# Optimization experiments

Measured on AMD Instinct MI355X. Metric: run time of the kernel, lower is better.

## Reference

```python
import jax, jax.numpy as jnp
import numpy as np

VOCAB = 50257
CUTOFF = (10000, 50000, 50257)  # cutoff + [vocab_size] per __init__
D = 1024
B, T = 2, 1024
HEAD_SZ = CUTOFF[0] + 2  # cutoff[0] + n_tail_clusters


def setup_inputs() -> dict:
    key = jax.random.key(0)
    ks = jax.random.split(key, 7)
    def xavier(k, shp):
        # xavier_uniform as in init_weights
        bound = np.sqrt(6.0 / (shp[0] + shp[1])).astype(np.float32)
        return jax.random.uniform(k, shp, dtype=jnp.float32, minval=-bound, maxval=bound)
    return {
        "input": jax.random.normal(ks[0], (B, T, D), dtype=jnp.float32),
        "target": jax.random.randint(ks[1], (B, T), 0, VOCAB),
        "head_w": xavier(ks[2], (HEAD_SZ, D)),              # [10002, 1024]
        "t0_a": xavier(ks[3], (D, D)),                       # [1024, 1024]
        "t0_b": xavier(ks[4], (CUTOFF[1] - CUTOFF[0], D)),   # [40000, 1024]
        "t1_a": xavier(ks[5], (D // 4, D)),                  # [256, 1024]
        "t1_b": xavier(ks[6], (CUTOFF[2] - CUTOFF[1], D // 4)),  # [207, 256]
    }


def reference(input, target, head_w, t0_a, t0_b, t1_a, t1_b):
    # Faithful jax version of AdaptiveSoftmax.get_log_prob (eval mode, dropout=0).
    # Torch updates log_probs[idxs, start:end] only for rows whose target lies in
    # cluster i (leaving other rows zero); we express the same gather->small GEMM
    # chain->log_softmax->prior-add->scatter via masked writes (jit-friendly).
    bsz, length, dim = input.shape
    xi = input.reshape(-1, dim)                     # [N, D]
    tgt = target.reshape(-1)                        # [N]

    head_lp = jax.nn.log_softmax(xi @ head_w.T, axis=1)        # [N, HEAD_SZ]
    tail_priors = head_lp[:, CUTOFF[0] - 1:HEAD_SZ - 1]        # [N, 2]

    log_probs = jnp.zeros((xi.shape[0], VOCAB), dtype=input.dtype)
    log_probs = log_probs.at[:, :HEAD_SZ].set(head_lp)

    tails = ((t0_a, t0_b), (t1_a, t1_b))
    for i, (wa, wb) in enumerate(tails):
        lo, hi = CUTOFF[i], CUTOFF[i + 1]
        mask = (tgt >= lo) & (tgt < hi)                        # [N]
        # Linear(D, D//4**i) -> Linear(D//4**i, hi-lo), then log_softmax + prior
        tail_lp = jax.nn.log_softmax((xi @ wa.T) @ wb.T, axis=1) + tail_priors[:, i:i + 1]
        log_probs = log_probs.at[:, lo:hi].set(
            jnp.where(mask[:, None], tail_lp, log_probs[:, lo:hi]))
    return log_probs.reshape(bsz, length, VOCAB)
```

## Files before the change

### kernel.cpp

```cpp
#include <hip/hip_runtime.h>

typedef unsigned short u16;
typedef unsigned int u32;
typedef __attribute__((ext_vector_type(4))) float f32x4;
typedef __bf16 bf16x8 __attribute__((ext_vector_type(8)));
typedef __attribute__((ext_vector_type(8))) unsigned short u16x8;

__device__ __forceinline__ u16 f2bf(float x) {
    u32 u = __builtin_bit_cast(u32, x);
    u += 0x7FFFu + ((u >> 16) & 1u);
    return (u16)(u >> 16);
}
__device__ __forceinline__ float bf2f(u16 u) {
    return __builtin_bit_cast(float, ((u32)u) << 16);
}
__device__ __forceinline__ void gld_lds16(void* lds, const void* g) {
    __builtin_amdgcn_global_load_lds(
        (const __attribute__((address_space(1))) void*)g,
        (__attribute__((address_space(3))) void*)lds, 16, 0, 0);
}

__device__ __forceinline__ size_t pack_base_tail(long row) {
    return (size_t)row * 100514 + 59936 - ((row * 2) & 7);
}
__device__ __forceinline__ size_t pack_base_head(long row) {
    return (size_t)row * 100514 + 20480 - ((row * 2) & 7);
}

__global__ __launch_bounds__(256) void cvt_all(const float* __restrict__ x,
                                               const float* __restrict__ hw,
                                               const float* __restrict__ t0a,
                                               const float* __restrict__ t1a,
                                               const float* __restrict__ t0b,
                                               const float* __restrict__ t1b,
                                               u16* __restrict__ XI, u16* __restrict__ HW,
                                               u16* __restrict__ TAB, u16* __restrict__ T0B,
                                               u16* __restrict__ T1B) {
    int b = blockIdx.x;
    const float* src; u16* dst; int n, b0, nb;
    if (b < 80)        { src = x;    dst = XI;            n = 2097152;  b0 = 0;    nb = 80;   }
    else if (b < 472)  { src = hw;   dst = HW;            n = 10242048; b0 = 80;   nb = 392;  }
    else if (b < 512)  { src = t0a;  dst = TAB;           n = 1048576;  b0 = 472;  nb = 40;   }
    else if (b < 522)  { src = t1a;  dst = TAB + 1048576; n = 262144;   b0 = 512;  nb = 10;   }
    else if (b < 2086) { src = t0b;  dst = T0B;           n = 40960000; b0 = 522;  nb = 1564; }
    else if (b < 2090) { src = t1b;  dst = T1B;           n = 65792;    b0 = 2086; nb = 4;    }
    else if (b < 2100) { src = 0;    dst = HW + 10242048; n = 243712;   b0 = 2090; nb = 10;   }
    else               { src = 0;    dst = T0B + 40960000; n = 196608;  b0 = 2100; nb = 8;    }
    int i0 = (b - b0) * 1024 + threadIdx.x * 4;
    int stride = nb * 1024;
    if (src) {
        for (int i = i0; i < n; i += stride) {
            float4 v = *(const float4*)(src + i);
            ushort4 o;
            o.x = f2bf(v.x); o.y = f2bf(v.y); o.z = f2bf(v.z); o.w = f2bf(v.w);
            *(ushort4*)(dst + i) = o;
        }
    } else {
        ushort4 z = {0, 0, 0, 0};
        for (int i = i0; i < n; i += stride) *(ushort4*)(dst + i) = z;
    }
}

__global__ __launch_bounds__(256) void build_map(const int* __restrict__ tgt,
                                                 int* __restrict__ rowlist,
                                                 int* __restrict__ cntbuf) {
    __shared__ int cs[257];
    __shared__ int fu[256];
    int t = threadIdx.x;
    int cnt_local = 0, first_un = 1 << 30;
    int mk[8];
#pragma unroll
    for (int k = 0; k < 8; k++) {
        int r = t * 8 + k;
        int tg = tgt[r];
        int m = (tg >= 10000 && tg < 50000) ? 1 : 0;
        mk[k] = m;
        cnt_local += m;
        if (!m && first_un == (1 << 30)) first_un = r;
    }
    cs[t + 1] = cnt_local;
    fu[t] = first_un;
    __syncthreads();
    if (t == 0) {
        cs[0] = 0;
        for (int i = 1; i <= 256; i++) cs[i] += cs[i - 1];
        int d = 1 << 30;
        for (int i = 0; i < 256; i++) d = min(d, fu[i]);
        if (d == (1 << 30)) d = 0;
        int cnt = cs[256];
        cntbuf[0] = cnt;
        cntbuf[1] = (cnt + 255) & ~255;
        cntbuf[2] = d;
    }
    __syncthreads();
    int off = cs[t];
#pragma unroll
    for (int k = 0; k < 8; k++)
        if (mk[k]) rowlist[off++] = t * 8 + k;
    int cnt = cs[256], cntp = (cnt + 255) & ~255, d = cntbuf[2];
    for (int j = cnt + t; j < cntp; j += 256) rowlist[j] = d;
}

template <int TAIL>
__global__ __launch_bounds__(512, 2) void gemm256(const u16* __restrict__ A,
                                                  const u16* __restrict__ B,
                                                  u16* __restrict__ outpk,
                                                  const int* __restrict__ rowlist,
                                                  const int* __restrict__ cntbuf,
                                                  float* __restrict__ part) {
    const int m0 = blockIdx.x * 256, n0 = blockIdx.y * 256;
    if (TAIL) { if (m0 >= cntbuf[1]) return; }
    __shared__ u16 lds[4][16384];
    const int tid = threadIdx.x;
    const int lane = tid & 63, wv = tid >> 6;
    const int wm = wv >> 2, wn = wv & 3;
    const int lr = lane & 15, hi = lane >> 4;

    const int c0 = tid, c1 = 512 + tid;
    int ga0 = m0 + ((c0 >> 6) << 4) + (c0 & 15);
    int ga1 = m0 + ((c1 >> 6) << 4) + (c1 & 15);
    const u16* sA0;
    const u16* sA1;
    if (TAIL) {
        sA0 = A + (size_t)rowlist[ga0] * 1280 + ((c0 >> 4) & 3) * 8;
        sA1 = A + (size_t)rowlist[ga1] * 1280 + ((c1 >> 4) & 3) * 8;
    } else {
        sA0 = A + (size_t)ga0 * 1024 + ((c0 >> 4) & 3) * 8;
        sA1 = A + (size_t)ga1 * 1024 + ((c1 >> 4) & 3) * 8;
    }
    const u16* sB0 = B + (size_t)(n0 + ((c0 >> 6) << 4) + (c0 & 15)) * 1024 + ((c0 >> 4) & 3) * 8;
    const u16* sB1 = B + (size_t)(n0 + ((c1 >> 6) << 4) + (c1 & 15)) * 1024 + ((c1 >> 4) & 3) * 8;

    f32x4 acc[8][4] = {};

    auto stage = [&](int buf, int kt) {
        char* d = (char*)&lds[buf][0] + tid * 16;
        gld_lds16(d,          sA0 + kt);
        gld_lds16(d + 8192,   sA1 + kt);
        gld_lds16(d + 16384,  sB0 + kt);
        gld_lds16(d + 24576,  sB1 + kt);
    };
    auto compute = [&](int buf) {
        const u16* LA = &lds[buf][0];
        const u16* LB = &lds[buf][8192];
        bf16x8 bfr[4];
#pragma unroll
        for (int j = 0; j < 4; j++)
            bfr[j] = *(const bf16x8*)(LB + (wn * 4 + j) * 512 + hi * 128 + lr * 8);
        __builtin_amdgcn_s_setprio(1);
#pragma unroll
        for (int m = 0; m < 8; m++) {
            bf16x8 af = *(const bf16x8*)(LA + (wm * 8 + m) * 512 + hi * 128 + lr * 8);
#pragma unroll
            for (int j = 0; j < 4; j++)
                acc[m][j] = __builtin_amdgcn_mfma_f32_16x16x32_bf16(af, bfr[j], acc[m][j], 0, 0, 0);
        }
        __builtin_amdgcn_s_setprio(0);
    };

    stage(0, 0);
    stage(1, 32);
    asm volatile("s_waitcnt vmcnt(4)" ::: "memory");
    __builtin_amdgcn_s_barrier();
#pragma unroll 1
    for (int t = 0; t < 30; ++t) {
        stage((t + 2) & 3, (t + 2) * 32);
        compute(t & 3);
        asm volatile("s_waitcnt vmcnt(4)" ::: "memory");
        __builtin_amdgcn_s_barrier();
    }
    compute(2);
    asm volatile("s_waitcnt vmcnt(0)" ::: "memory");
    __builtin_amdgcn_s_barrier();
    compute(3);

    const int cr = hi * 4, cc = lr;
    const int climit = TAIL ? 40000 : 10002;
    const int pstride = TAIL ? 628 : 160;
#pragma unroll
    for (int m = 0; m < 8; m++) {
#pragma unroll
        for (int q = 0; q < 4; q++) {
            int r = m0 + wm * 128 + m * 16 + cr + q;
            long orow = TAIL ? rowlist[r] : r;
            size_t base = TAIL ? pack_base_tail(orow) : pack_base_head(orow);
            u16* dst = outpk + base + n0 + wn * 64 + cc;
            float s = 0.f;
#pragma unroll
            for (int j = 0; j < 4; j++) {
                float v = acc[m][j][q];
                dst[j * 16] = f2bf(v);
                int col = n0 + wn * 64 + j * 16 + cc;
                s += (col < climit) ? __expf(v) : 0.f;
            }
            s += __shfl_xor(s, 1); s += __shfl_xor(s, 2);
            s += __shfl_xor(s, 4); s += __shfl_xor(s, 8);
            if (cc == 0) part[(size_t)r * pstride + (n0 >> 6) + wn] = s;
        }
    }
}

__global__ __launch_bounds__(256) void gemm_nt_bf16(const u16* __restrict__ A, int lda,
                                                    const u16* __restrict__ B, int ldb,
                                                    u16* __restrict__ Cb, long ldc, int K) {
    __shared__ u16 lA[128 * 32];
    __shared__ u16 lB[128 * 32];
    const int tid = threadIdx.x;
    const int lane = tid & 63, wv = tid >> 6;
    const int m0 = blockIdx.x * 128, n0 = blockIdx.y * 128;

    const u16* gA0 = A + (size_t)(m0 + (tid >> 2)) * lda + (tid & 3) * 8;
    const u16* gB0 = B + (size_t)(n0 + (tid >> 2)) * ldb + (tid & 3) * 8;
    char* dA = (char*)lA + wv * 1024;
    char* dB = (char*)lB + wv * 1024;

    f32x4 acc[4][4] = {};
    const int wm = wv >> 1, wn = wv & 1;
    const int lr = lane & 15;
    const int lk = (lane >> 4) * 8;

    for (int kt = 0; kt < K; kt += 32) {
        __syncthreads();
        gld_lds16(dA, gA0);
        gld_lds16(dA + 4096, gA0 + 64 * (size_t)lda);
        gld_lds16(dB, gB0);
        gld_lds16(dB + 4096, gB0 + 64 * (size_t)ldb);
        gA0 += 32; gB0 += 32;
        __syncthreads();

        bf16x8 af[4], bfr[4];
#pragma unroll
        for (int i = 0; i < 4; i++) {
            af[i]  = *(const bf16x8*)(lA + (wm * 64 + i * 16 + lr) * 32 + lk);
            bfr[i] = *(const bf16x8*)(lB + (wn * 64 + i * 16 + lr) * 32 + lk);
        }
#pragma unroll
        for (int i = 0; i < 4; i++)
#pragma unroll
            for (int j = 0; j < 4; j++)
                acc[i][j] = __builtin_amdgcn_mfma_f32_16x16x32_bf16(af[i], bfr[j], acc[i][j], 0, 0, 0);
    }

    const int cr = (lane >> 4) * 4;
    const int cc = lane & 15;
#pragma unroll
    for (int i = 0; i < 4; i++) {
        int rbase = m0 + wm * 64 + i * 16 + cr;
#pragma unroll
        for (int j = 0; j < 4; j++) {
            int c = n0 + wn * 64 + j * 16 + cc;
#pragma unroll
            for (int q = 0; q < 4; q++)
                Cb[(size_t)(rbase + q) * (size_t)ldc + c] = f2bf(acc[i][j][q]);
        }
    }
}

__global__ __launch_bounds__(256) void head_norm(float* __restrict__ out,
                                                 float* __restrict__ stats,
                                                 const float* __restrict__ parth) {
    const int row = blockIdx.x, tid = threadIdx.x;
    float s = (tid < 160) ? parth[(size_t)row * 160 + tid] : 0.f;
#pragma unroll
    for (int o = 32; o; o >>= 1) s += __shfl_xor(s, o);
    __shared__ float red[4];
    if ((tid & 63) == 0) red[tid >> 6] = s;
    __syncthreads();
    float logZ = __logf(red[0] + red[1] + red[2] + red[3]);
    const u16* pk = (const u16*)out + pack_base_head(row);
    float* p = out + (size_t)row * 50257;
    for (int k = 0; k < 5; k++) {
        int c0 = k * 2048 + tid * 8;
        if (c0 + 8 <= 10002) {
            u16x8 xv = *(const u16x8*)(pk + c0);
#pragma unroll
            for (int z = 0; z < 8; z++) p[c0 + z] = bf2f(xv[z]) - logZ;
        } else if (c0 < 10002) {
            for (int z = 0; c0 + z < 10002; z++) p[c0 + z] = bf2f(pk[c0 + z]) - logZ;
        }
    }
    if (tid == 0) {
        float* st = stats + row * 8;
        float l0 = bf2f(pk[9999]) - logZ;
        float l1 = bf2f(pk[10000]) - logZ;
        float l2 = bf2f(pk[10001]) - logZ;
        st[0] = l0; st[1] = l1; st[2] = l1; st[3] = l2;
    }
}

__global__ __launch_bounds__(256) void reduce_t0(const float* __restrict__ part,
                                                 const int* __restrict__ rowlist,
                                                 const int* __restrict__ cntbuf,
                                                 const float* __restrict__ ST,
                                                 float* __restrict__ FA) {
    int r = blockIdx.x;
    if (r >= cntbuf[0]) return;
    int tid = threadIdx.x;
    float s = 0.f;
    for (int c = tid; c < 628; c += 256) s += part[(size_t)r * 628 + c];
#pragma unroll
    for (int o = 32; o; o >>= 1) s += __shfl_xor(s, o);
    __shared__ float red[4];
    if ((tid & 63) == 0) red[tid >> 6] = s;
    __syncthreads();
    if (tid == 0) {
        float S = red[0] + red[1] + red[2] + red[3];
        int orow = rowlist[r];
        FA[orow] = __logf(S) - ST[orow * 8 + 0];
    }
}

__global__ __launch_bounds__(256) void tail0_norm(float* __restrict__ out,
                                                  const int* __restrict__ tgt,
                                                  const float* __restrict__ ST,
                                                  const float* __restrict__ FA) {
    const int row = blockIdx.x, tid = threadIdx.x;
    float* p = out + (size_t)row * 50257 + 10000;
    int t = tgt[row];
    if (t >= 10000 && t < 50000) {
        float A = FA[row];
        const u16* src = (const u16*)out + pack_base_tail(row);
        for (int k = 0; k < 5; k++) {
            float v[4][8];
#pragma unroll
            for (int g = 0; g < 4; g++) {
                int o = 2048 * g + tid * 8;
                if (o < 8000) {
                    u16x8 xv = *(const u16x8*)(src + 8000 * k + o);
#pragma unroll
                    for (int z = 0; z < 8; z++) v[g][z] = bf2f(xv[z]);
                }
            }
            __syncthreads();
#pragma unroll
            for (int g = 0; g < 4; g++) {
                int o = 2048 * g + tid * 8;
                if (o < 8000) {
                    int e = 8000 * k + o;
#pragma unroll
                    for (int z = 0; z < 8; z++) p[e + z] = v[g][z] - A;
                }
            }
            __syncthreads();
        }
    } else {
        float v0 = ST[row * 8 + 2], v1 = ST[row * 8 + 3];
        for (int e = tid; e < 40000; e += 256) p[e] = 0.f;
        if (tid == 0) { p[0] = v0; p[1] = v1; }
    }
}

__global__ __launch_bounds__(256) void tail1_kernel(float* __restrict__ out,
                                                    const int* __restrict__ tgt,
                                                    const u16* __restrict__ proj,
                                                    const u16* __restrict__ t1b,
                                                    const float* __restrict__ stats) {
    const int row = blockIdx.x, tid = threadIdx.x;
    float* p = out + (size_t)row * 50257 + 50000;
    int t = tgt[row];
    if (t < 50000) {
        for (int c = tid; c < 257; c += 256) p[c] = 0.f;
        return;
    }
    __shared__ float pr[256];
    __shared__ float lg[257];
    __shared__ float red[4];
    pr[tid] = bf2f(proj[(size_t)row * 1280 + 1024 + tid]);
    __syncthreads();
    for (int c = tid; c < 257; c += 256) {
        const u16* w = t1b + c * 256;
        float acc = 0.f;
        for (int k = 0; k < 256; k++) acc += bf2f(w[k]) * pr[k];
        lg[c] = acc;
    }
    __syncthreads();
    float s = 0.f;
    for (int c = tid; c < 257; c += 256) s += __expf(lg[c]);
#pragma unroll
    for (int o = 32; o; o >>= 1) s += __shfl_xor(s, o);
    if ((tid & 63) == 0) red[tid >> 6] = s;
    __syncthreads();
    float A = __logf(red[0] + red[1] + red[2] + red[3]) - stats[row * 8 + 1];
    for (int c = tid; c < 257; c += 256) p[c] = lg[c] - A;
}

#define OFF_XI    0UL
#define OFF_HEADW 4194304UL
#define OFF_TAB   25165824UL
#define OFF_T0B   27787264UL
#define OFF_T1B   110100480UL
#define OFF_PROJ  110232064UL
#define OFF_ST    115474944UL
#define OFF_PART  115540480UL
#define OFF_PARTH 120685056UL
#define OFF_FA    121995776UL
#define OFF_MAP   122003968UL
#define OFF_CNT   122012160UL

extern "C" void kernel_launch(void* const* d_in, const int* in_sizes, int n_in,
                              void* d_out, int out_size, void* d_ws, size_t ws_size,
                              hipStream_t stream) {
    const float* x   = (const float*)d_in[0];
    const int*   tgt = (const int*)d_in[1];
    const float* hw  = (const float*)d_in[2];
    const float* t0a = (const float*)d_in[3];
    const float* t0b = (const float*)d_in[4];
    const float* t1a = (const float*)d_in[5];
    const float* t1b = (const float*)d_in[6];
    float* out = (float*)d_out;
    char* ws = (char*)d_ws;

    u16* XI     = (u16*)(ws + OFF_XI);
    u16* HW     = (u16*)(ws + OFF_HEADW);
    u16* TAB    = (u16*)(ws + OFF_TAB);
    u16* T0B    = (u16*)(ws + OFF_T0B);
    u16* T1B    = (u16*)(ws + OFF_T1B);
    u16* PROJ   = (u16*)(ws + OFF_PROJ);
    float* ST   = (float*)(ws + OFF_ST);
    float* PART = (float*)(ws + OFF_PART);
    float* PARTH = (float*)(ws + OFF_PARTH);
    float* FA   = (float*)(ws + OFF_FA);
    int* MAP    = (int*)(ws + OFF_MAP);
    int* CNT    = (int*)(ws + OFF_CNT);

    cvt_all<<<2108, 256, 0, stream>>>(x, hw, t0a, t1a, t0b, t1b, XI, HW, TAB, T0B, T1B);

    build_map<<<1, 256, 0, stream>>>(tgt, MAP, CNT);

    gemm256<0><<<dim3(8, 40), 512, 0, stream>>>(XI, HW, (u16*)d_out, nullptr, nullptr, PARTH);

    head_norm<<<2048, 256, 0, stream>>>(out, ST, PARTH);

    gemm_nt_bf16<<<dim3(16, 10), 256, 0, stream>>>(XI, 1024, TAB, 1024, PROJ, 1280L, 1024);

    gemm256<1><<<dim3(8, 157), 512, 0, stream>>>(PROJ, T0B, (u16*)d_out, MAP, CNT, PART);

    reduce_t0<<<2048, 256, 0, stream>>>(PART, MAP, CNT, ST, FA);
    tail0_norm<<<2048, 256, 0, stream>>>(out, tgt, ST, FA);

    tail1_kernel<<<2048, 256, 0, stream>>>(out, tgt, PROJ, T1B, ST);
}
```

Baseline: 558.1 us.

## Interleave LDS reads, global loads and MFMA phases; fuse tail0 reduce into norm

The GEMM main loop is split into two half-phases, each fenced by scheduling barriers. A and B tile loads are issued separately and interleaved with LDS fragment reads and MFMA groups, so memory traffic overlaps compute at a finer grain. The build_map kernel now lists all rows, masked rows first and unmasked rows after, in place of padding with a dummy row. This lets reduce_t0 be merged into tail0_norm, which indexes through the row list and drops one launch and the FA buffer. The extra barriers add synchronisation points and the register pressure may change.

```diff
diff --git a/kernel.cpp b/kernel.cpp
--- a/kernel.cpp
+++ b/kernel.cpp
@@ -65,41 +65,35 @@
                                                  int* __restrict__ rowlist,
                                                  int* __restrict__ cntbuf) {
     __shared__ int cs[257];
-    __shared__ int fu[256];
     int t = threadIdx.x;
-    int cnt_local = 0, first_un = 1 << 30;
+    int cnt_local = 0;
     int mk[8];
 #pragma unroll
     for (int k = 0; k < 8; k++) {
-        int r = t * 8 + k;
-        int tg = tgt[r];
-        int m = (tg >= 10000 && tg < 50000) ? 1 : 0;
-        mk[k] = m;
-        cnt_local += m;
-        if (!m && first_un == (1 << 30)) first_un = r;
+        int tg = tgt[t * 8 + k];
+        mk[k] = (tg >= 10000 && tg < 50000) ? 1 : 0;
+        cnt_local += mk[k];
     }
     cs[t + 1] = cnt_local;
-    fu[t] = first_un;
     __syncthreads();
     if (t == 0) {
         cs[0] = 0;
         for (int i = 1; i <= 256; i++) cs[i] += cs[i - 1];
-        int d = 1 << 30;
-        for (int i = 0; i < 256; i++) d = min(d, fu[i]);
-        if (d == (1 << 30)) d = 0;
-        int cnt = cs[256];
-        cntbuf[0] = cnt;
-        cntbuf[1] = (cnt + 255) & ~255;
-        cntbuf[2] = d;
-    }
-    __syncthreads();
-    int off = cs[t];
-#pragma unroll
-    for (int k = 0; k < 8; k++)
-        if (mk[k]) rowlist[off++] = t * 8 + k;
-    int cnt = cs[256], cntp = (cnt + 255) & ~255, d = cntbuf[2];
-    for (int j = cnt + t; j < cntp; j += 256) rowlist[j] = d;
-}
+        cntbuf[0] = cs[256];
+        cntbuf[1] = (cs[256] + 255) & ~255;
+    }
+    __syncthreads();
+    int cnt = cs[256];
+    int offm = cs[t];
+    int offu = cnt + (t * 8 - cs[t]);
+#pragma unroll
+    for (int k = 0; k < 8; k++) {
+        if (mk[k]) rowlist[offm++] = t * 8 + k;
+        else       rowlist[offu++] = t * 8 + k;
+    }
+}
+
+#define PH_BAR() do { __builtin_amdgcn_sched_barrier(0); __builtin_amdgcn_s_barrier(); __builtin_amdgcn_sched_barrier(0); } while (0)
 
 template <int TAIL>
 __global__ __launch_bounds__(512, 2) void gemm256(const u16* __restrict__ A,
@@ -132,47 +126,82 @@
     const u16* sB1 = B + (size_t)(n0 + ((c1 >> 6) << 4) + (c1 & 15)) * 1024 + ((c1 >> 4) & 3) * 8;
 
     f32x4 acc[8][4] = {};
-
-    auto stage = [&](int buf, int kt) {
+    bf16x8 Bf[4], Af[4];
+
+    auto stageA = [&](int buf, int kt) {
         char* d = (char*)&lds[buf][0] + tid * 16;
-        gld_lds16(d,          sA0 + kt);
-        gld_lds16(d + 8192,   sA1 + kt);
-        gld_lds16(d + 16384,  sB0 + kt);
-        gld_lds16(d + 24576,  sB1 + kt);
+        gld_lds16(d,        sA0 + kt);
+        gld_lds16(d + 8192, sA1 + kt);
     };
-    auto compute = [&](int buf) {
-        const u16* LA = &lds[buf][0];
-        const u16* LB = &lds[buf][8192];
-        bf16x8 bfr[4];
+    auto stageB = [&](int buf, int kt) {
+        char* d = (char*)&lds[buf][0] + tid * 16;
+        gld_lds16(d + 16384, sB0 + kt);
+        gld_lds16(d + 24576, sB1 + kt);
+    };
+    auto readB = [&](const u16* L) {
 #pragma unroll
         for (int j = 0; j < 4; j++)
-            bfr[j] = *(const bf16x8*)(LB + (wn * 4 + j) * 512 + hi * 128 + lr * 8);
+            Bf[j] = *(const bf16x8*)(L + 8192 + (wn * 4 + j) * 512 + hi * 128 + lr * 8);
+    };
+    auto readA = [&](const u16* L, int q) {
+#pragma unroll
+        for (int m = 0; m < 4; m++)
+            Af[m] = *(const bf16x8*)(L + (wm * 8 + q * 4 + m) * 512 + hi * 128 + lr * 8);
+    };
+    auto mfma16 = [&](int q) {
         __builtin_amdgcn_s_setprio(1);
 #pragma unroll
-        for (int m = 0; m < 8; m++) {
-            bf16x8 af = *(const bf16x8*)(LA + (wm * 8 + m) * 512 + hi * 128 + lr * 8);
+        for (int m = 0; m < 4; m++)
 #pragma unroll
             for (int j = 0; j < 4; j++)
-                acc[m][j] = __builtin_amdgcn_mfma_f32_16x16x32_bf16(af, bfr[j], acc[m][j], 0, 0, 0);
-        }
+                acc[q * 4 + m][j] = __builtin_amdgcn_mfma_f32_16x16x32_bf16(Af[m], Bf[j], acc[q * 4 + m][j], 0, 0, 0);
         __builtin_amdgcn_s_setprio(0);
     };
 
-    stage(0, 0);
-    stage(1, 32);
+    stageA(0, 0);  stageB(0, 0);
+    stageA(1, 32); stageB(1, 32);
     asm volatile("s_waitcnt vmcnt(4)" ::: "memory");
     __builtin_amdgcn_s_barrier();
+    __builtin_amdgcn_sched_barrier(0);
+
 #pragma unroll 1
     for (int t = 0; t < 30; ++t) {
-        stage((t + 2) & 3, (t + 2) * 32);
-        compute(t & 3);
+        const u16* L = &lds[t & 3][0];
+        const int b2 = (t + 2) & 3, kt2 = (t + 2) * 32;
+        readB(L); readA(L, 0);
+        stageA(b2, kt2);
+        PH_BAR();
+        mfma16(0);
+        PH_BAR();
+        readA(L, 1);
+        stageB(b2, kt2);
         asm volatile("s_waitcnt vmcnt(4)" ::: "memory");
-        __builtin_amdgcn_s_barrier();
-    }
-    compute(2);
-    asm volatile("s_waitcnt vmcnt(0)" ::: "memory");
-    __builtin_amdgcn_s_barrier();
-    compute(3);
+        PH_BAR();
+        mfma16(1);
+        PH_BAR();
+    }
+    {
+        const u16* L = &lds[2][0];
+        readB(L); readA(L, 0);
+        PH_BAR();
+        mfma16(0);
+        PH_BAR();
+        readA(L, 1);
+        asm volatile("s_waitcnt vmcnt(0)" ::: "memory");
+        PH_BAR();
+        mfma16(1);
+        PH_BAR();
+    }
+    {
+        const u16* L = &lds[3][0];
+        readB(L); readA(L, 0);
+        PH_BAR();
+        mfma16(0);
+        PH_BAR();
+        readA(L, 1);
+        __builtin_amdgcn_sched_barrier(0);
+        mfma16(1);
+    }
 
     const int cr = hi * 4, cc = lr;
     const int climit = TAIL ? 40000 : 10002;
@@ -288,37 +317,24 @@
     }
 }
 
-__global__ __launch_bounds__(256) void reduce_t0(const float* __restrict__ part,
-                                                 const int* __restrict__ rowlist,
-                                                 const int* __restrict__ cntbuf,
-                                                 const float* __restrict__ ST,
-                                                 float* __restrict__ FA) {
-    int r = blockIdx.x;
-    if (r >= cntbuf[0]) return;
-    int tid = threadIdx.x;
-    float s = 0.f;
-    for (int c = tid; c < 628; c += 256) s += part[(size_t)r * 628 + c];
-#pragma unroll
-    for (int o = 32; o; o >>= 1) s += __shfl_xor(s, o);
+__global__ __launch_bounds__(256) void tail0_norm(float* __restrict__ out,
+                                                  const int* __restrict__ rowlist,
+                                                  const int* __restrict__ cntbuf,
+                                                  const float* __restrict__ ST,
+                                                  const float* __restrict__ PART) {
+    const int b = blockIdx.x, tid = threadIdx.x;
+    const int cnt = cntbuf[0];
+    const long row = rowlist[b];
+    float* p = out + (size_t)row * 50257 + 10000;
     __shared__ float red[4];
-    if ((tid & 63) == 0) red[tid >> 6] = s;
-    __syncthreads();
-    if (tid == 0) {
-        float S = red[0] + red[1] + red[2] + red[3];
-        int orow = rowlist[r];
-        FA[orow] = __logf(S) - ST[orow * 8 + 0];
-    }
-}
-
-__global__ __launch_bounds__(256) void tail0_norm(float* __restrict__ out,
-                                                  const int* __restrict__ tgt,
-                                                  const float* __restrict__ ST,
-                                                  const float* __restrict__ FA) {
-    const int row = blockIdx.x, tid = threadIdx.x;
-    float* p = out + (size_t)row * 50257 + 10000;
-    int t = tgt[row];
-    if (t >= 10000 && t < 50000) {
-        float A = FA[row];
+    if (b < cnt) {
+        float s = 0.f;
+        for (int c = tid; c < 628; c += 256) s += PART[(size_t)b * 628 + c];
+#pragma unroll
+        for (int o = 32; o; o >>= 1) s += __shfl_xor(s, o);
+        if ((tid & 63) == 0) red[tid >> 6] = s;
+        __syncthreads();
+        float Aa = __logf(red[0] + red[1] + red[2] + red[3]) - ST[row * 8 + 0];
         const u16* src = (const u16*)out + pack_base_tail(row);
         for (int k = 0; k < 5; k++) {
             float v[4][8];
@@ -338,7 +354,7 @@
                 if (o < 8000) {
                     int e = 8000 * k + o;
 #pragma unroll
-                    for (int z = 0; z < 8; z++) p[e + z] = v[g][z] - A;
+                    for (int z = 0; z < 8; z++) p[e + z] = v[g][z] - Aa;
                 }
             }
             __syncthreads();
@@ -393,9 +409,8 @@
 #define OFF_ST    115474944UL
 #define OFF_PART  115540480UL
 #define OFF_PARTH 120685056UL
-#define OFF_FA    121995776UL
-#define OFF_MAP   122003968UL
-#define OFF_CNT   122012160UL
+#define OFF_MAP   121995776UL
+#define OFF_CNT   122003968UL
 
 extern "C" void kernel_launch(void* const* d_in, const int* in_sizes, int n_in,
                               void* d_out, int out_size, void* d_ws, size_t ws_size,
@@ -419,7 +434,6 @@
     float* ST   = (float*)(ws + OFF_ST);
     float* PART = (float*)(ws + OFF_PART);
     float* PARTH = (float*)(ws + OFF_PARTH);
-    float* FA   = (float*)(ws + OFF_FA);
     int* MAP    = (int*)(ws + OFF_MAP);
     int* CNT    = (int*)(ws + OFF_CNT);
 
@@ -435,8 +449,7 @@
 
     gemm256<1><<<dim3(8, 157), 512, 0, stream>>>(PROJ, T0B, (u16*)d_out, MAP, CNT, PART);
 
-    reduce_t0<<<2048, 256, 0, stream>>>(PART, MAP, CNT, ST, FA);
-    tail0_norm<<<2048, 256, 0, stream>>>(out, tgt, ST, FA);
+    tail0_norm<<<2048, 256, 0, stream>>>(out, MAP, CNT, ST, PART);
 
     tail1_kernel<<<2048, 256, 0, stream>>>(out, tgt, PROJ, T1B, ST);
 }
```

After: 577.4 us. +3.5%, slower.
